# Performance work log

Hardware: AMD Instinct MI355X
Metric: run time of the kernel (lower is better)

## Reference

```python
import jax, jax.numpy as jnp
import numpy as np

H = 1024          # hidden_size
NH = 16           # num_heads = hidden_size // head_dim
DK = 64           # head_dim (key)
DV = 64           # head_v_dim
VDIM = 1024       # value_dim
DECAY_LR, GATE_LR, A_LR, V_LR = 64, 160, 64, 64
W_SCALE = -0.6065306597126334  # -exp(-0.5)
GN_EPS = 64 * 1e-5             # head_dim * norm_eps


def _lora(x, A, B, b, act):
    h = x @ A.T
    if act is not None:
        h = act(h)
    y = h @ B.T
    return y if b is None else y + b


def setup_inputs() -> dict:
    key = jax.random.key(0)
    ks = iter(jax.random.split(key, 40))
    def n(shape, s=0.02):
        return jax.random.normal(next(ks), shape, dtype=jnp.float32) * s
    inp = {
        'hidden_states': jax.random.normal(next(ks), (8, 2048, H), jnp.float32),
        'v_first': jax.random.normal(next(ks), (8, 2048, VDIM), jnp.float32),
        'x_r': n((1, 1, H), 0.5), 'x_w': n((1, 1, H), 0.5), 'x_k': n((1, 1, H), 0.5),
        'x_v': n((1, 1, H), 0.5), 'x_a': n((1, 1, H), 0.5), 'x_g': n((1, 1, H), 0.5),
        'k_k': 0.71 + n((H,), 0.05),
        'k_a': 1.02 + n((H,), 0.05),
        'r_k': -0.04 + n((NH, DK), 0.05),
        'W_r': n((H, H)), 'W_k': n((H, H)), 'W_v': n((VDIM, H)), 'W_o': n((H, VDIM)),
        'w_lora_A': n((DECAY_LR, H)), 'w_lora_B': n((H, DECAY_LR)), 'w_lora_b': n((H,), 0.5) - 4.0,
        'a_lora_A': n((A_LR, H)), 'a_lora_B': n((H, A_LR)), 'a_lora_b': n((H,), 0.1),
        'v_lora_A': n((V_LR, H)), 'v_lora_B': n((VDIM, V_LR)), 'v_lora_b': 0.73 + n((VDIM,), 0.1),
        'g_lora_A': n((GATE_LR, H)), 'g_lora_B': n((VDIM, GATE_LR)),
        'gn_w': jnp.ones((VDIM,), jnp.float32), 'gn_b': jnp.zeros((VDIM,), jnp.float32),
    }
    return inp


def reference(hidden_states, v_first, x_r, x_w, x_k, x_v, x_a, x_g, k_k, k_a, r_k,
              W_r, W_k, W_v, W_o, w_lora_A, w_lora_B, w_lora_b,
              a_lora_A, a_lora_B, a_lora_b, v_lora_A, v_lora_B, v_lora_b,
              g_lora_A, g_lora_B, gn_w, gn_b):
    x = hidden_states
    B_, T, _ = x.shape
    # token shift: delta[t] = x[t-1] - x[t], x[-1] = 0
    shifted = jnp.pad(x, ((0, 0), (1, 0), (0, 0)))[:, :T]
    delta = shifted - x
    xr = x + delta * x_r; xw = x + delta * x_w; xk = x + delta * x_k
    xv = x + delta * x_v; xa = x + delta * x_a; xg = x + delta * x_g

    r = xr @ W_r.T
    w = W_SCALE * jax.nn.sigmoid(_lora(xw, w_lora_A, w_lora_B, w_lora_b, jnp.tanh))  # log-decay in (-e^-0.5, 0)
    k = xk @ W_k.T
    v = xv @ W_v.T
    v = v + (v_first - v) * jax.nn.sigmoid(_lora(xv, v_lora_A, v_lora_B, v_lora_b, None))  # layer_idx != 0
    a = jax.nn.sigmoid(_lora(xa, a_lora_A, a_lora_B, a_lora_b, None))
    g = _lora(xg, g_lora_A, g_lora_B, None, jax.nn.sigmoid)

    kk = (k * k_k).reshape(B_, T, NH, DK)
    kk = kk / jnp.maximum(jnp.linalg.norm(kk, axis=-1, keepdims=True), 1e-12)  # l2 norm per head
    k = k * (1.0 + (a - 1.0) * k_a)

    rh = r.reshape(B_, T, NH, DK)
    wh = w.reshape(B_, T, NH, DK)
    kh = k.reshape(B_, T, NH, DK)
    vh = v.reshape(B_, T, NH, DV)
    ah = -kk                               # delta-rule 'a' (removal direction)
    bh = kk * a.reshape(B_, T, NH, DK)     # delta-rule 'b' (write direction)

    def step(S, inputs):
        # S: [B, H, DK, DV]; inputs each [B, H, D]
        r_t, w_t, k_t, v_t, a_t, b_t = inputs
        sa = jnp.einsum('bhk,bhkv->bhv', a_t, S)
        S = S * jnp.exp(w_t)[..., None] \
            + jnp.einsum('bhk,bhv->bhkv', b_t, sa) \
            + jnp.einsum('bhk,bhv->bhkv', k_t, v_t)
        o_t = jnp.einsum('bhk,bhkv->bhv', r_t, S)
        return S, o_t

    seq = tuple(jnp.moveaxis(t, 1, 0) for t in (rh, wh, kh, vh, ah, bh))  # [T,B,H,D]
    S0 = jnp.zeros((B_, NH, DK, DV), dtype=x.dtype)
    _, o = jax.lax.scan(step, S0, seq)
    o = jnp.moveaxis(o, 0, 1)  # [B, T, NH, DV]

    # GroupNorm with num_groups = num_heads over value_dim channels == per-head LayerNorm (no per-head affine)
    mu = o.mean(-1, keepdims=True)
    var = o.var(-1, keepdims=True)
    on = ((o - mu) / jnp.sqrt(var + GN_EPS)).reshape(B_, T, VDIM) * gn_w + gn_b

    bonus = ((rh * kh * r_k).sum(-1, keepdims=True) * vh).reshape(B_, T, VDIM)
    out = ((on + bonus) * g) @ W_o.T
    return out
```

## Files before the change

### kernel.cpp

```cpp
#include <hip/hip_runtime.h>
#include <hip/hip_bf16.h>


#define DEVI __device__ __forceinline__

constexpr int TSEQ = 2048;
constexpr int HID  = 1024;
constexpr int BTOT = 16384;
constexpr int CCH  = 32;
constexpr int NCH  = TSEQ / CCH;
constexpr int L4N  = 352;
constexpr float W_SCALE = -0.6065306597126334f;
constexpr float GN_EPS  = 6.4e-4f;

using s16x8  = __attribute__((ext_vector_type(8))) short;
using f32x4v = __attribute__((ext_vector_type(4))) float;

DEVI float4 ld4(const float* p) { return *reinterpret_cast<const float4*>(p); }
DEVI void   st4(float* p, float4 v) { *reinterpret_cast<float4*>(p) = v; }
DEVI float  sigf(float x) { return 1.0f / (1.0f + __expf(-x)); }
DEVI unsigned short bfr(float f) {
    unsigned int u = __float_as_uint(f);
    return (unsigned short)((u + 0x7fffu + ((u >> 16) & 1u)) >> 16);
}
DEVI float bff(unsigned short s) { return __uint_as_float(((unsigned int)s) << 16); }
DEVI unsigned int pk2(float lo, float hi) {
    return ((unsigned int)bfr(hi) << 16) | (unsigned int)bfr(lo);
}
DEVI void up8(uint4 u, float* f) {
    f[0]=bff((unsigned short)(u.x & 0xffffu)); f[1]=bff((unsigned short)(u.x >> 16));
    f[2]=bff((unsigned short)(u.y & 0xffffu)); f[3]=bff((unsigned short)(u.y >> 16));
    f[4]=bff((unsigned short)(u.z & 0xffffu)); f[5]=bff((unsigned short)(u.z >> 16));
    f[6]=bff((unsigned short)(u.w & 0xffffu)); f[7]=bff((unsigned short)(u.w >> 16));
}
DEVI f32x4v MF(s16x8 a, s16x8 b, f32x4v c) {
    return __builtin_amdgcn_mfma_f32_16x16x32_bf16(a, b, c, 0, 0, 0);
}
DEVI void gl16(const void* g, void* l) {
    __builtin_amdgcn_global_load_lds(
        (const __attribute__((address_space(1))) unsigned int*)g,
        (__attribute__((address_space(3))) unsigned int*)l, 16, 0, 0);
}
DEVI void gl4(const void* g, void* l) {
    __builtin_amdgcn_global_load_lds(
        (const __attribute__((address_space(1))) unsigned int*)g,
        (__attribute__((address_space(3))) unsigned int*)l, 4, 0, 0);
}

struct CastArgs {
    const float* src[12];
    unsigned short* dst[12];
    int start4[13];
};
__global__ __launch_bounds__(256) void cast_all_kernel(CastArgs a) {
    int i4 = blockIdx.x * 256 + threadIdx.x;
    if (i4 >= a.start4[12]) return;
    int seg = 0;
#pragma unroll
    for (int s = 1; s < 12; s++) seg += (i4 >= a.start4[s]) ? 1 : 0;
    int off = (i4 - a.start4[seg]) * 4;
    float4 v = ld4(a.src[seg] + off);
    ushort4 o; o.x = bfr(v.x); o.y = bfr(v.y); o.z = bfr(v.z); o.w = bfr(v.w);
    *reinterpret_cast<ushort4*>(a.dst[seg] + off) = o;
}

__global__ __launch_bounds__(256) void proj3_kernel(
        const float* __restrict__ x,
        const float* __restrict__ cr, const float* __restrict__ ck,
        const float* __restrict__ cv,
        const unsigned short* __restrict__ Wr, const unsigned short* __restrict__ Wk,
        const unsigned short* __restrict__ Wv,
        unsigned short* __restrict__ Ro, unsigned short* __restrict__ Ko,
        unsigned short* __restrict__ Vo) {
    __shared__ __align__(16) unsigned short As[3][64 * 32];
    __shared__ __align__(16) unsigned short Bs[3][128 * 32];
    const int tid = threadIdx.x;
    const int w = tid >> 6, l = tid & 63;
    const int bm = blockIdx.x * 64, bn = blockIdx.y * 128;
    const int wm = w >> 1, wn = w & 1;
    const int lr = l & 15, lq = l >> 4, lk = lq * 8;

    f32x4v acc[3][2][4];
#pragma unroll
    for (int p = 0; p < 3; p++)
#pragma unroll
        for (int i = 0; i < 2; i++)
#pragma unroll
            for (int j = 0; j < 4; j++)
#pragma unroll
                for (int q = 0; q < 4; q++) acc[p][i][j][q] = 0.f;

    const float* cvs[3] = {cr, ck, cv};
    const unsigned short* Ws[3] = {Wr, Wk, Wv};

    for (int k0 = 0; k0 < HID; k0 += 32) {
        {
            const int row = tid >> 2, kp = (tid & 3) * 8;
            const int gr = bm + row;
            const float* xp = x + (size_t)gr * HID + k0 + kp;
            float4 x0 = ld4(xp), x1 = ld4(xp + 4);
            float4 p0 = make_float4(0.f, 0.f, 0.f, 0.f), p1 = p0;
            if ((gr & (TSEQ - 1)) != 0) { p0 = ld4(xp - HID); p1 = ld4(xp - HID + 4); }
            float xb[8] = {x0.x, x0.y, x0.z, x0.w, x1.x, x1.y, x1.z, x1.w};
            float dx[8] = {p0.x - x0.x, p0.y - x0.y, p0.z - x0.z, p0.w - x0.w,
                           p1.x - x1.x, p1.y - x1.y, p1.z - x1.z, p1.w - x1.w};
#pragma unroll
            for (int p = 0; p < 3; p++) {
                float4 c0 = ld4(cvs[p] + k0 + kp), c1 = ld4(cvs[p] + k0 + kp + 4);
                float cc[8] = {c0.x, c0.y, c0.z, c0.w, c1.x, c1.y, c1.z, c1.w};
                uint4 u;
                u.x = pk2(fmaf(dx[0], cc[0], xb[0]), fmaf(dx[1], cc[1], xb[1]));
                u.y = pk2(fmaf(dx[2], cc[2], xb[2]), fmaf(dx[3], cc[3], xb[3]));
                u.z = pk2(fmaf(dx[4], cc[4], xb[4]), fmaf(dx[5], cc[5], xb[5]));
                u.w = pk2(fmaf(dx[6], cc[6], xb[6]), fmaf(dx[7], cc[7], xb[7]));
                *reinterpret_cast<uint4*>(&As[p][row * 32 + kp]) = u;
            }
        }
#pragma unroll
        for (int p = 0; p < 3; p++)
#pragma unroll
            for (int c = 0; c < 2; c++) {
                int idx = c * 256 + tid;
                int rw = idx >> 2, kp2 = (idx & 3) * 8;
                gl16(Ws[p] + (size_t)(bn + rw) * HID + k0 + kp2,
                     &Bs[p][c * 2048 + w * 512]);
            }
        __syncthreads();
#pragma unroll
        for (int p = 0; p < 3; p++) {
            s16x8 af[2], bf4[4];
#pragma unroll
            for (int i = 0; i < 2; i++)
                af[i] = *reinterpret_cast<const s16x8*>(
                    &As[p][(wm * 32 + i * 16 + lr) * 32 + lk]);
#pragma unroll
            for (int j = 0; j < 4; j++)
                bf4[j] = *reinterpret_cast<const s16x8*>(
                    &Bs[p][(wn * 64 + j * 16 + lr) * 32 + lk]);
#pragma unroll
            for (int i = 0; i < 2; i++)
#pragma unroll
                for (int j = 0; j < 4; j++)
                    acc[p][i][j] = MF(af[i], bf4[j], acc[p][i][j]);
        }
        __syncthreads();
    }

    unsigned short* dsts[3] = {Ro, Ko, Vo};
#pragma unroll
    for (int p = 0; p < 3; p++)
#pragma unroll
        for (int i = 0; i < 2; i++)
#pragma unroll
            for (int j = 0; j < 4; j++)
#pragma unroll
                for (int q = 0; q < 4; q++) {
                    const int grow = bm + wm * 32 + i * 16 + lq * 4 + q;
                    const int gcol = bn + wn * 64 + j * 16 + lr;
                    dsts[p][(size_t)grow * HID + gcol] = bfr(acc[p][i][j][q]);
                }
}

__global__ __launch_bounds__(256) void lora4_kernel(
        const float* __restrict__ x,
        const float* __restrict__ cv_, const float* __restrict__ cw_,
        const float* __restrict__ ca_, const float* __restrict__ cg_,
        const unsigned short* __restrict__ LW, unsigned short* __restrict__ H1) {
    __shared__ __align__(16) unsigned short As[4][64 * 32];
    __shared__ __align__(16) unsigned short Bs[L4N * 32];
    const int tid = threadIdx.x;
    const int w = tid >> 6, l = tid & 63;
    const int lr = l & 15, lq = l >> 4, lk = lq * 8;
    const int bm = blockIdx.x * 64;
    const float* cvs[4] = {cv_, cw_, ca_, cg_};

    f32x4v acc[22];
#pragma unroll
    for (int j = 0; j < 22; j++)
#pragma unroll
        for (int q = 0; q < 4; q++) acc[j][q] = 0.f;

    for (int k0 = 0; k0 < HID; k0 += 32) {
        {
            const int row = tid >> 2, kp = (tid & 3) * 8;
            const int gr = bm + row;
            const float* xp = x + (size_t)gr * HID + k0 + kp;
            float4 x0 = ld4(xp), x1 = ld4(xp + 4);
            float4 p0 = make_float4(0.f, 0.f, 0.f, 0.f), p1 = p0;
            if ((gr & (TSEQ - 1)) != 0) { p0 = ld4(xp - HID); p1 = ld4(xp - HID + 4); }
            float xb[8] = {x0.x, x0.y, x0.z, x0.w, x1.x, x1.y, x1.z, x1.w};
            float dx[8] = {p0.x - x0.x, p0.y - x0.y, p0.z - x0.z, p0.w - x0.w,
                           p1.x - x1.x, p1.y - x1.y, p1.z - x1.z, p1.w - x1.w};
#pragma unroll
            for (int p = 0; p < 4; p++) {
                float4 c0 = ld4(cvs[p] + k0 + kp), c1 = ld4(cvs[p] + k0 + kp + 4);
                float cc[8] = {c0.x, c0.y, c0.z, c0.w, c1.x, c1.y, c1.z, c1.w};
                uint4 u;
                u.x = pk2(fmaf(dx[0], cc[0], xb[0]), fmaf(dx[1], cc[1], xb[1]));
                u.y = pk2(fmaf(dx[2], cc[2], xb[2]), fmaf(dx[3], cc[3], xb[3]));
                u.z = pk2(fmaf(dx[4], cc[4], xb[4]), fmaf(dx[5], cc[5], xb[5]));
                u.w = pk2(fmaf(dx[6], cc[6], xb[6]), fmaf(dx[7], cc[7], xb[7]));
                *reinterpret_cast<uint4*>(&As[p][row * 32 + kp]) = u;
            }
        }
#pragma unroll
        for (int c = 0; c < 6; c++) {
            int idx = c * 256 + tid;
            if (idx < L4N * 4) {
                gl16(LW + (size_t)(idx >> 2) * HID + (idx & 3) * 8 + k0,
                     (char*)&Bs[0] + (c * 256 + w * 64) * 16);
            }
        }
        __syncthreads();
        s16x8 af[4];
#pragma unroll
        for (int p = 0; p < 4; p++)
            af[p] = *reinterpret_cast<const s16x8*>(&As[p][(w * 16 + lr) * 32 + lk]);
#pragma unroll
        for (int j = 0; j < 22; j++) {
            const int grp = (j < 4) ? 0 : (j < 8) ? 1 : (j < 12) ? 2 : 3;
            s16x8 bf = *reinterpret_cast<const s16x8*>(&Bs[(j * 16 + lr) * 32 + lk]);
            acc[j] = MF(af[grp], bf, acc[j]);
        }
        __syncthreads();
    }

#pragma unroll
    for (int j = 0; j < 22; j++)
#pragma unroll
        for (int q = 0; q < 4; q++) {
            const int grow = bm + w * 16 + lq * 4 + q;
            const int gcol = j * 16 + lr;
            float d = acc[j][q];
            if (j >= 4 && j < 8) d = tanhf(d);
            else if (j >= 12) d = sigf(d);
            H1[(size_t)grow * L4N + gcol] = bfr(d);
        }
}

__global__ __launch_bounds__(256) void stage2_kernel(
        const unsigned short* __restrict__ H1,
        const unsigned short* __restrict__ vB16, const unsigned short* __restrict__ wB16,
        const unsigned short* __restrict__ aB16,
        const float* __restrict__ vb, const float* __restrict__ wb,
        const float* __restrict__ ab,
        unsigned short* __restrict__ Vout, unsigned short* __restrict__ Wout,
        unsigned short* __restrict__ Aout,
        const unsigned short* __restrict__ aux1, const float* __restrict__ aux2) {
    const int z = blockIdx.z;
    const unsigned short* Bw = (z == 0) ? vB16 : (z == 1) ? wB16 : aB16;
    const float* bias = (z == 0) ? vb : (z == 1) ? wb : ab;
    unsigned short* Cout = (z == 0) ? Vout : (z == 1) ? Wout : Aout;
    const int aoff = z * 64;
    __shared__ __align__(16) unsigned short As[128 * 32];
    __shared__ __align__(16) unsigned short Bs[128 * 32];
    const int tid = threadIdx.x;
    const int w = tid >> 6, l = tid & 63;
    const int bm = blockIdx.x * 128, bn = blockIdx.y * 128;
    const int wm = w >> 1, wn = w & 1;
    const int lr = l & 15, lk = (l >> 4) * 8;

    f32x4v acc[4][4];
#pragma unroll
    for (int i = 0; i < 4; i++)
#pragma unroll
        for (int j = 0; j < 4; j++)
#pragma unroll
            for (int q = 0; q < 4; q++) acc[i][j][q] = 0.f;

    for (int k0 = 0; k0 < 64; k0 += 32) {
#pragma unroll
        for (int c = 0; c < 2; c++) {
            int idx = c * 256 + tid;
            int row = idx >> 2, kp = (idx & 3) * 8;
            gl16(H1 + (size_t)(bm + row) * L4N + aoff + k0 + kp,
                 &As[c * 2048 + w * 512]);
        }
#pragma unroll
        for (int c = 0; c < 2; c++) {
            int idx = c * 256 + tid;
            int row = idx >> 2, kp = (idx & 3) * 8;
            gl16(Bw + (size_t)(bn + row) * 64 + k0 + kp, &Bs[c * 2048 + w * 512]);
        }
        __syncthreads();
        s16x8 afx[4], bfx[4];
#pragma unroll
        for (int i = 0; i < 4; i++)
            afx[i] = *reinterpret_cast<const s16x8*>(&As[(wm * 64 + i * 16 + lr) * 32 + lk]);
#pragma unroll
        for (int j = 0; j < 4; j++)
            bfx[j] = *reinterpret_cast<const s16x8*>(&Bs[(wn * 64 + j * 16 + lr) * 32 + lk]);
#pragma unroll
        for (int i = 0; i < 4; i++)
#pragma unroll
            for (int j = 0; j < 4; j++)
                acc[i][j] = MF(afx[i], bfx[j], acc[i][j]);
        __syncthreads();
    }

#pragma unroll
    for (int i = 0; i < 4; i++) {
        const int grow0 = bm + wm * 64 + i * 16 + (l >> 4) * 4;
#pragma unroll
        for (int j = 0; j < 4; j++) {
            const int gcol = bn + wn * 64 + j * 16 + lr;
            const float bsv = bias[gcol];
#pragma unroll
            for (int q = 0; q < 4; q++) {
                const int grow = grow0 + q;
                float d = acc[i][j][q];
                if (z == 0) {
                    float v0 = bff(aux1[(size_t)grow * HID + gcol]);
                    d = fmaf(aux2[(size_t)grow * HID + gcol] - v0, sigf(d + bsv), v0);
                } else if (z == 1) {
                    d = W_SCALE * sigf(d + bsv);
                } else {
                    d = sigf(d + bsv);
                }
                Cout[(size_t)grow * HID + gcol] = bfr(d);
            }
        }
    }
}

template<int BM, int BN, int MODE, bool OUTBF>
__global__ __launch_bounds__(256) void mgemm(
        const unsigned short* __restrict__ Ab, const unsigned short* __restrict__ Bw,
        void* Cout, int N, int K, int lda,
        const float* __restrict__ bias,
        const unsigned short* aux1, const float* __restrict__ aux2) {
    constexpr int BK = 32;
    constexpr int WM_ = (BN == 128) ? 2 : 4;
    constexpr int WN_ = (BN == 128) ? 2 : 1;
    constexpr int WTM = BM / WM_, WTN = BN / WN_;
    constexpr int MF_ = WTM / 16, NF = WTN / 16;
    constexpr int ACALLS = (BM * BK) / 2048;
    constexpr int BCALLS = (BN * BK) / 2048;
    __shared__ __align__(16) unsigned short As[BM * BK];
    __shared__ __align__(16) unsigned short Bs[BN * BK];
    const int tid = threadIdx.x;
    const int w = tid >> 6, l = tid & 63;
    const int bm = blockIdx.x * BM, bn = blockIdx.y * BN;
    const int wm = w / WN_, wn = w % WN_;
    const int lr = l & 15, lk = (l >> 4) * 8;

    f32x4v acc[MF_][NF];
#pragma unroll
    for (int i = 0; i < MF_; i++)
#pragma unroll
        for (int j = 0; j < NF; j++)
#pragma unroll
            for (int q = 0; q < 4; q++) acc[i][j][q] = 0.f;

    for (int k0 = 0; k0 < K; k0 += BK) {
#pragma unroll
        for (int c = 0; c < ACALLS; c++) {
            int idx = c * 256 + tid;
            int row = idx >> 2, kp = (idx & 3) * 8;
            gl16(Ab + (size_t)(bm + row) * lda + k0 + kp, &As[c * 2048 + w * 512]);
        }
#pragma unroll
        for (int c = 0; c < BCALLS; c++) {
            int idx = c * 256 + tid;
            int row = idx >> 2, kp = (idx & 3) * 8;
            int gc = bn + row; if (gc > N - 1) gc = N - 1;
            gl16(Bw + (size_t)gc * K + k0 + kp, &Bs[c * 2048 + w * 512]);
        }
        __syncthreads();
        s16x8 afx[MF_], bfx[NF];
#pragma unroll
        for (int i = 0; i < MF_; i++)
            afx[i] = *reinterpret_cast<const s16x8*>(&As[(wm * WTM + i * 16 + lr) * BK + lk]);
#pragma unroll
        for (int j = 0; j < NF; j++)
            bfx[j] = *reinterpret_cast<const s16x8*>(&Bs[(wn * WTN + j * 16 + lr) * BK + lk]);
#pragma unroll
        for (int i = 0; i < MF_; i++)
#pragma unroll
            for (int j = 0; j < NF; j++)
                acc[i][j] = __builtin_amdgcn_mfma_f32_16x16x32_bf16(
                    afx[i], bfx[j], acc[i][j], 0, 0, 0);
        __syncthreads();
    }

#pragma unroll
    for (int i = 0; i < MF_; i++) {
        const int grow0 = bm + wm * WTM + i * 16 + (l >> 4) * 4;
#pragma unroll
        for (int j = 0; j < NF; j++) {
            const int gcol = bn + wn * WTN + j * 16 + lr;
            if (gcol >= N) continue;
#pragma unroll
            for (int q = 0; q < 4; q++) {
                const int grow = grow0 + q;
                float d = acc[i][j][q];
                if (OUTBF) ((unsigned short*)Cout)[(size_t)grow * N + gcol] = bfr(d);
                else       ((float*)Cout)[(size_t)grow * N + gcol] = d;
            }
        }
    }
}

__global__ __launch_bounds__(64) void cprep_kernel(
        unsigned short* __restrict__ K16, unsigned short* __restrict__ A16,
        unsigned short* __restrict__ R16, unsigned short* __restrict__ KK16,
        const unsigned short* __restrict__ W16,
        const float* __restrict__ kkc, const float* __restrict__ kac,
        const float* __restrict__ rkw,
        float* __restrict__ SB, float* __restrict__ Ed,
        unsigned short* __restrict__ MvH, unsigned short* __restrict__ MvL) {
    __shared__ __align__(16) unsigned short sA[32][64], sB[32][64], sK[32][64];
    __shared__ __align__(16) unsigned short AtT[64][40];
    __shared__ __align__(16) float Mab[32][36];
    __shared__ __align__(16) unsigned short MnvH[32][40], MnvL[32][40];
    __shared__ __align__(16) unsigned short MakTH[32][40], MakTL[32][40];
    const int bid = blockIdx.x;
    const int bh = bid >> 6, ch = bid & 63;
    const int bb = bh >> 4, hh = bh & 15;
    const int l = threadIdx.x;
    const int chn = hh * 64 + l;
    const float kkcv = kkc[chn], kacv = kac[chn], rkv = rkw[chn];
    const size_t cbase = ((size_t)(bb * TSEQ) + ch * CCH) * HID + hh * 64;
    size_t off = cbase + l;
    float cw = 0.f, er = 1.f;
    for (int i = 0; i < CCH; i++, off += HID) {
        const float k = bff(K16[off]);
        const float a = bff(A16[off]);
        const float r = bff(R16[off]);
        const float wv = bff(W16[off]);
        const float kr = k * kkcv;
        float ss = kr * kr;
        ss += __shfl_xor(ss, 1);  ss += __shfl_xor(ss, 2);
        ss += __shfl_xor(ss, 4);  ss += __shfl_xor(ss, 8);
        ss += __shfl_xor(ss, 16); ss += __shfl_xor(ss, 32);
        const float inv = 1.0f / fmaxf(sqrtf(ss), 1e-12f);
        const float kk = kr * inv;
        const float b  = kk * a;
        const float kn = k * fmaf(a - 1.0f, kacv, 1.0f);
        float s3 = r * kn * rkv;
        s3 += __shfl_xor(s3, 1);  s3 += __shfl_xor(s3, 2);
        s3 += __shfl_xor(s3, 4);  s3 += __shfl_xor(s3, 8);
        s3 += __shfl_xor(s3, 16); s3 += __shfl_xor(s3, 32);
        if (l == 0) SB[(size_t)bh * TSEQ + ch * CCH + i] = s3;
        const float cwp = cw; cw += wv;
        const float ea = __expf(cwp), ei = __expf(-cw);
        er = __expf(cw);
        const unsigned short At = bfr(-kk * ea);
        const unsigned short Bt = bfr(b * ei);
        const unsigned short Kt = bfr(kn * ei);
        A16[off] = Bt;
        K16[off] = Kt;
        R16[off] = bfr(r * er);
        sA[i][l] = At; sB[i][l] = Bt; sK[i][l] = Kt;
        AtT[l][i] = At;
    }
    Ed[((size_t)bh * NCH + ch) * 64 + l] = er;
    __syncthreads();
    const int lr = l & 15, lq = l >> 4;
    f32x4v z4; z4[0] = z4[1] = z4[2] = z4[3] = 0.f;
#pragma unroll
    for (int mi = 0; mi < 2; mi++)
#pragma unroll
        for (int ni = 0; ni < 2; ni++) {
            s16x8 a0 = *reinterpret_cast<const s16x8*>(&sA[mi * 16 + lr][lq * 8]);
            s16x8 a1 = *reinterpret_cast<const s16x8*>(&sA[mi * 16 + lr][32 + lq * 8]);
            s16x8 b0 = *reinterpret_cast<const s16x8*>(&sB[ni * 16 + lr][lq * 8]);
            s16x8 b1 = *reinterpret_cast<const s16x8*>(&sB[ni * 16 + lr][32 + lq * 8]);
            s16x8 k0 = *reinterpret_cast<const s16x8*>(&sK[ni * 16 + lr][lq * 8]);
            s16x8 k1 = *reinterpret_cast<const s16x8*>(&sK[ni * 16 + lr][32 + lq * 8]);
            f32x4v m  = MF(a1, b1, MF(a0, b0, z4));
            f32x4v mk = MF(a1, k1, MF(a0, k0, z4));
#pragma unroll
            for (int q = 0; q < 4; q++) {
                int r = mi * 16 + lq * 4 + q, cc2 = ni * 16 + lr;
                Mab[r][cc2] = (cc2 < r) ? m[q] : 0.f;
                float vv = (cc2 < r) ? mk[q] : 0.f;
                unsigned short h = bfr(vv);
                MakTH[cc2][r] = h;
                MakTL[cc2][r] = bfr(vv - bff(h));
            }
        }
    __syncthreads();
    const int j = l & 31;
    float m[32];
#pragma unroll
    for (int i = 0; i < 32; i++) m[i] = (i == j) ? 1.f : 0.f;
#pragma unroll
    for (int i = 1; i < 32; i++) {
        float p0 = 0.f, p1 = 0.f, p2 = 0.f, p3 = 0.f;
#pragma unroll
        for (int k4_ = 0; k4_ < 32; k4_ += 4) {
            if (k4_ >= i) break;
            float4 L4 = *reinterpret_cast<const float4*>(&Mab[i][k4_]);
            p0 = fmaf(L4.x, m[k4_ + 0], p0);
            if (k4_ + 1 < i) p1 = fmaf(L4.y, m[k4_ + 1], p1);
            if (k4_ + 2 < i) p2 = fmaf(L4.z, m[k4_ + 2], p2);
            if (k4_ + 3 < i) p3 = fmaf(L4.w, m[k4_ + 3], p3);
        }
        m[i] += (p0 + p1) + (p2 + p3);
    }
    if (l < 32) {
#pragma unroll
        for (int i = 0; i < 32; i++) {
            unsigned short h = bfr(m[i]);
            MnvH[i][j] = h;
            MnvL[i][j] = bfr(m[i] - bff(h));
        }
    }
    __syncthreads();
    {
        unsigned short* dH = MvH + (size_t)(bh * NCH + ch) * 1024;
        unsigned short* dL = MvL + (size_t)(bh * NCH + ch) * 1024;
#pragma unroll
        for (int mi = 0; mi < 2; mi++) {
            s16x8 ah = *reinterpret_cast<const s16x8*>(&MnvH[mi * 16 + lr][lq * 8]);
            s16x8 al = *reinterpret_cast<const s16x8*>(&MnvL[mi * 16 + lr][lq * 8]);
#pragma unroll
            for (int n = 0; n < 4; n++) {
                s16x8 bt = *reinterpret_cast<const s16x8*>(&AtT[n * 16 + lr][lq * 8]);
                f32x4v am = MF(al, bt, MF(ah, bt, z4));
#pragma unroll
                for (int q = 0; q < 4; q++)
                    KK16[cbase + (size_t)(mi * 16 + lq * 4 + q) * HID + n * 16 + lr]
                        = bfr(am[q]);
            }
#pragma unroll
            for (int n = 0; n < 2; n++) {
                s16x8 mh = *reinterpret_cast<const s16x8*>(&MakTH[n * 16 + lr][lq * 8]);
                s16x8 ml = *reinterpret_cast<const s16x8*>(&MakTL[n * 16 + lr][lq * 8]);
                f32x4v lm = MF(ah, ml, MF(al, mh, MF(ah, mh, z4)));
#pragma unroll
                for (int q = 0; q < 4; q++) {
                    const int r = mi * 16 + lq * 4 + q, cc = n * 16 + lr;
                    unsigned short h = bfr(lm[q]);
                    dH[r * 32 + cc] = h;
                    dL[r * 32 + cc] = bfr(lm[q] - bff(h));
                }
            }
        }
    }
}

__global__ __launch_bounds__(256) void recchunk_kernel(
        const unsigned short* __restrict__ AMG, const unsigned short* __restrict__ BtG,
        const unsigned short* __restrict__ KtG, const unsigned short* __restrict__ RtG,
        const unsigned short* __restrict__ V16, const float* __restrict__ Ed,
        const unsigned short* __restrict__ LMH, const unsigned short* __restrict__ LML,
        unsigned short* __restrict__ Ob16) {
    __shared__ __align__(16) unsigned short stT[2][4][CCH][64];
    __shared__ __align__(16) unsigned short stMh[2][32][32], stMl[2][32][32];
    __shared__ __align__(16) unsigned short stV[2][CCH][16];
    __shared__ __align__(16) float stEd[2][64];
    __shared__ __align__(16) unsigned short Shi[16][74], Slo[16][74];
    __shared__ __align__(16) unsigned short BtT[64][42], KtT[64][42];
    __shared__ __align__(16) unsigned short VT[16][42];
    __shared__ __align__(16) unsigned short MrkH[32][42], MrkL[32][42];
    __shared__ __align__(16) unsigned short MrbH[32][42], MrbL[32][42];
    __shared__ __align__(16) unsigned short SATh[16][42], SATl[16][42];

    const int bid = blockIdx.x;
    const int vq = bid >> 7, bh = bid & 127;
    const int tid = threadIdx.x;
    const int w = tid >> 6, l = tid & 63;
    const int lr = l & 15, lq = l >> 4;
    const int bb = bh >> 4, hh = bh & 15;
    const size_t rowoff = ((size_t)bb * TSEQ) * HID + hh * 64;
    const int mi = w >> 1, ni = w & 1;

    const int r8 = l >> 3, ck = l & 7;
    const int swz8 = (ck ^ r8) * 8;

    auto STAGE = [&](int buf, int cn) {
        if (cn >= NCH) return;
        const size_t cb = rowoff + (size_t)(cn * CCH) * HID;
        const unsigned short* srcs[4] = {AMG, BtG, KtG, RtG};
        const unsigned short* T = srcs[w];
#pragma unroll
        for (int c = 0; c < 4; c++)
            gl16(T + cb + (size_t)(c * 8 + r8) * HID + swz8, &stT[buf][w][c * 8][0]);
        if (w == 0) {
            gl16(V16 + cb + (size_t)(l >> 1) * HID + vq * 16 + (l & 1) * 8,
                 &stV[buf][0][0]);
            gl4(Ed + ((size_t)bh * NCH + cn) * 64 + l, &stEd[buf][0]);
        } else if (w == 1) {
#pragma unroll
            for (int c = 0; c < 2; c++)
                gl16(LMH + (size_t)(bh * NCH + cn) * 1024 + c * 512 + l * 8,
                     (char*)&stMh[buf][0][0] + c * 1024);
        } else if (w == 2) {
#pragma unroll
            for (int c = 0; c < 2; c++)
                gl16(LML + (size_t)(bh * NCH + cn) * 1024 + c * 512 + l * 8,
                     (char*)&stMl[buf][0][0] + c * 1024);
        }
    };

    for (int idx = tid; idx < 16 * 74; idx += 256) {
        ((unsigned short*)Shi)[idx] = 0;
        ((unsigned short*)Slo)[idx] = 0;
    }
    STAGE(0, 0);
    asm volatile("s_waitcnt vmcnt(0)" ::: "memory");
    __syncthreads();

    auto fragT = [&](int bf, int tn, int rbase, int kb) -> s16x8 {
        int row = rbase + lr;
        int chv = ((kb >> 3) + lq) ^ (row & 7);
        return *reinterpret_cast<const s16x8*>(
            (const char*)&stT[bf][tn][0][0] + row * 128 + chv * 16);
    };
    auto fragS = [&](const unsigned short (*Sx)[74], int kb) -> s16x8 {
        return *reinterpret_cast<const s16x8*>(&Sx[lr][kb + lq * 8]);
    };
    auto frag42 = [&](const unsigned short (*T)[42], int rbase) -> s16x8 {
        return *reinterpret_cast<const s16x8*>(&T[rbase + lr][lq * 8]);
    };

    f32x4v Sacc;
#pragma unroll
    for (int q = 0; q < 4; q++) Sacc[q] = 0.f;
    f32x4v z4; z4[0] = z4[1] = z4[2] = z4[3] = 0.f;

    int buf = 0;
    for (int c = 0; c < NCH; c++) {
        STAGE(buf ^ 1, c + 1);
        {
            const int tt = tid & 31, g8 = tid >> 5;
            const int ch = g8 ^ (tt & 7);
            uint4 bu = *reinterpret_cast<const uint4*>(&stT[buf][1][tt][ch * 8]);
            uint4 ku = *reinterpret_cast<const uint4*>(&stT[buf][2][tt][ch * 8]);
            unsigned int bw[4] = {bu.x, bu.y, bu.z, bu.w};
            unsigned int kw[4] = {ku.x, ku.y, ku.z, ku.w};
#pragma unroll
            for (int e = 0; e < 4; e++) {
                BtT[g8 * 8 + 2 * e][tt]     = (unsigned short)(bw[e] & 0xffffu);
                BtT[g8 * 8 + 2 * e + 1][tt] = (unsigned short)(bw[e] >> 16);
                KtT[g8 * 8 + 2 * e][tt]     = (unsigned short)(kw[e] & 0xffffu);
                KtT[g8 * 8 + 2 * e + 1][tt] = (unsigned short)(kw[e] >> 16);
            }
            if (g8 < 4) {
                ushort4 vu = *reinterpret_cast<const ushort4*>(&stV[buf][tt][g8 * 4]);
                VT[g8 * 4 + 0][tt] = vu.x; VT[g8 * 4 + 1][tt] = vu.y;
                VT[g8 * 4 + 2][tt] = vu.z; VT[g8 * 4 + 3][tt] = vu.w;
            }
        }
        __syncthreads();
        f32x4v oac = z4;
        if (ni == 0) {
            s16x8 rt0 = fragT(buf, 3, mi * 16, 0), rt1 = fragT(buf, 3, mi * 16, 32);
            s16x8 sh0 = fragS(Shi, 0), sh1 = fragS(Shi, 32);
            s16x8 sl0 = fragS(Slo, 0), sl1 = fragS(Slo, 32);
            oac = MF(rt1, sl1, MF(rt0, sl0, MF(rt1, sh1, MF(rt0, sh0, z4))));
#pragma unroll
            for (int n = 0; n < 2; n++) {
                s16x8 kt0 = fragT(buf, 2, n * 16, 0), kt1 = fragT(buf, 2, n * 16, 32);
                s16x8 bt0 = fragT(buf, 1, n * 16, 0), bt1 = fragT(buf, 1, n * 16, 32);
                f32x4v mrk = MF(rt1, kt1, MF(rt0, kt0, z4));
                f32x4v mrb = MF(rt1, bt1, MF(rt0, bt0, z4));
#pragma unroll
                for (int q = 0; q < 4; q++) {
                    const int r = mi * 16 + lq * 4 + q, cc = n * 16 + lr;
                    float vv = (cc <= r) ? mrk[q] : 0.f;
                    unsigned short h = bfr(vv);
                    MrkH[r][cc] = h; MrkL[r][cc] = bfr(vv - bff(h));
                    vv = (cc <= r) ? mrb[q] : 0.f; h = bfr(vv);
                    MrbH[r][cc] = h; MrbL[r][cc] = bfr(vv - bff(h));
                }
            }
        } else {
            s16x8 am0 = fragT(buf, 0, mi * 16, 0), am1 = fragT(buf, 0, mi * 16, 32);
            s16x8 sh0 = fragS(Shi, 0), sh1 = fragS(Shi, 32);
            s16x8 sl0 = fragS(Slo, 0), sl1 = fragS(Slo, 32);
            s16x8 vt0 = frag42(VT, 0);
            s16x8 lmh = *reinterpret_cast<const s16x8*>(&stMh[buf][mi * 16 + lr][lq * 8]);
            s16x8 lml = *reinterpret_cast<const s16x8*>(&stMl[buf][mi * 16 + lr][lq * 8]);
            f32x4v sat = MF(sl1, am1, MF(sl0, am0, MF(sh1, am1, MF(sh0, am0, z4))));
            sat = MF(vt0, lml, MF(vt0, lmh, sat));
#pragma unroll
            for (int q = 0; q < 4; q++) {
                const int r = lq * 4 + q, cc = mi * 16 + lr;
                unsigned short h = bfr(sat[q]);
                SATh[r][cc] = h;
                SATl[r][cc] = bfr(sat[q] - bff(h));
            }
        }
        __syncthreads();
        if (ni == 0) {
            s16x8 vt0 = frag42(VT, 0);
            oac = MF(frag42(MrkL, mi * 16), vt0,
                     MF(frag42(MrkH, mi * 16), vt0, oac));
            s16x8 sath = frag42(SATh, 0), satl = frag42(SATl, 0);
            s16x8 rbh = frag42(MrbH, mi * 16), rbl = frag42(MrbL, mi * 16);
            oac = MF(rbl, sath, MF(rbh, satl, MF(rbh, sath, oac)));
#pragma unroll
            for (int q = 0; q < 4; q++) {
                const int t = c * CCH + mi * 16 + lq * 4 + q;
                Ob16[rowoff + (size_t)t * HID + vq * 16 + lr] = bfr(oac[q]);
            }
        }
        {
            s16x8 sath = frag42(SATh, 0), satl = frag42(SATl, 0);
            s16x8 btf = frag42(BtT, w * 16);
            s16x8 ktf = frag42(KtT, w * 16);
            s16x8 vta = frag42(VT, 0);
            const float ed = stEd[buf][w * 16 + lr];
            Sacc = MF(sath, btf, Sacc);
            Sacc = MF(satl, btf, Sacc);
            Sacc = MF(vta, ktf, Sacc);
#pragma unroll
            for (int q = 0; q < 4; q++) {
                Sacc[q] *= ed;
                unsigned short h = bfr(Sacc[q]);
                Shi[lq * 4 + q][w * 16 + lr] = h;
                Slo[lq * 4 + q][w * 16 + lr] = bfr(Sacc[q] - bff(h));
            }
        }
        asm volatile("s_waitcnt vmcnt(0)" ::: "memory");
        __syncthreads();
        buf ^= 1;
    }
}

__global__ __launch_bounds__(256) void stats_kernel(
        const unsigned short* __restrict__ O16, float* __restrict__ MS) {
    const int row = blockIdx.x;
    const int tid = threadIdx.x;
    const int c = tid * 4;
    ushort4 ou = *reinterpret_cast<const ushort4*>(O16 + (size_t)row * HID + c);
    float o[4] = {bff(ou.x), bff(ou.y), bff(ou.z), bff(ou.w)};
    float s1 = o[0] + o[1] + o[2] + o[3];
    float s2 = o[0]*o[0] + o[1]*o[1] + o[2]*o[2] + o[3]*o[3];
#pragma unroll
    for (int m = 1; m < 16; m <<= 1) {
        s1 += __shfl_xor(s1, m); s2 += __shfl_xor(s2, m);
    }
    if ((tid & 15) == 0) {
        const int hh = tid >> 4;
        const float mu = s1 * (1.0f / 64.0f);
        const float var = s2 * (1.0f / 64.0f) - mu * mu;
        float2 v; v.x = mu; v.y = rsqrtf(var + GN_EPS);
        *reinterpret_cast<float2*>(MS + (size_t)row * 32 + hh * 2) = v;
    }
}

__global__ __launch_bounds__(256) void wogemm_kernel(
        const unsigned short* __restrict__ O16, const unsigned short* __restrict__ V16,
        const unsigned short* __restrict__ G16, const float* __restrict__ SB,
        const float* __restrict__ MS, const float* __restrict__ gnw,
        const float* __restrict__ gnb, const unsigned short* __restrict__ Wo,
        float* __restrict__ out) {
    __shared__ __align__(16) unsigned short As[128 * 32];
    __shared__ __align__(16) unsigned short Bs[128 * 32];
    const int tid = threadIdx.x;
    const int w = tid >> 6, l = tid & 63;
    const int bm = blockIdx.x * 128, bn = blockIdx.y * 128;
    const int wm = w >> 1, wn = w & 1;
    const int lr = l & 15, lk = (l >> 4) * 8;

    f32x4v acc[4][4];
#pragma unroll
    for (int i = 0; i < 4; i++)
#pragma unroll
        for (int j = 0; j < 4; j++)
#pragma unroll
            for (int q = 0; q < 4; q++) acc[i][j][q] = 0.f;

    for (int k0 = 0; k0 < HID; k0 += 32) {
#pragma unroll
        for (int c = 0; c < 2; c++) {
            int idx = c * 256 + tid;
            int row = idx >> 2, kp = (idx & 3) * 8;
            const int gr = bm + row;
            const size_t rb = (size_t)gr * HID + k0 + kp;
            uint4 ou = *reinterpret_cast<const uint4*>(O16 + rb);
            uint4 vu = *reinterpret_cast<const uint4*>(V16 + rb);
            uint4 gu = *reinterpret_cast<const uint4*>(G16 + rb);
            float o8[8], v8[8], g8[8];
            up8(ou, o8); up8(vu, v8); up8(gu, g8);
            const int hh = (k0 + kp) >> 6;
            float2 ms = *reinterpret_cast<const float2*>(MS + (size_t)gr * 32 + hh * 2);
            const float s3 = SB[((size_t)(gr >> 11) * 16 + hh) * TSEQ + (gr & (TSEQ - 1))];
            float4 w0 = ld4(gnw + k0 + kp), w1 = ld4(gnw + k0 + kp + 4);
            float4 b0 = ld4(gnb + k0 + kp), b1 = ld4(gnb + k0 + kp + 4);
            float wn8[8] = {w0.x, w0.y, w0.z, w0.w, w1.x, w1.y, w1.z, w1.w};
            float bn8[8] = {b0.x, b0.y, b0.z, b0.w, b1.x, b1.y, b1.z, b1.w};
            float y[8];
#pragma unroll
            for (int e = 0; e < 8; e++)
                y[e] = (fmaf((o8[e] - ms.x) * ms.y, wn8[e], bn8[e]) + s3 * v8[e]) * g8[e];
            uint4 u;
            u.x = pk2(y[0], y[1]); u.y = pk2(y[2], y[3]);
            u.z = pk2(y[4], y[5]); u.w = pk2(y[6], y[7]);
            *reinterpret_cast<uint4*>(&As[idx * 8]) = u;
        }
#pragma unroll
        for (int c = 0; c < 2; c++) {
            int idx = c * 256 + tid;
            int row = idx >> 2, kp = (idx & 3) * 8;
            gl16(Wo + (size_t)(bn + row) * HID + k0 + kp, &Bs[c * 2048 + w * 512]);
        }
        __syncthreads();
        s16x8 afx[4], bfx[4];
#pragma unroll
        for (int i = 0; i < 4; i++)
            afx[i] = *reinterpret_cast<const s16x8*>(&As[(wm * 64 + i * 16 + lr) * 32 + lk]);
#pragma unroll
        for (int j = 0; j < 4; j++)
            bfx[j] = *reinterpret_cast<const s16x8*>(&Bs[(wn * 64 + j * 16 + lr) * 32 + lk]);
#pragma unroll
        for (int i = 0; i < 4; i++)
#pragma unroll
            for (int j = 0; j < 4; j++)
                acc[i][j] = MF(afx[i], bfx[j], acc[i][j]);
        __syncthreads();
    }

#pragma unroll
    for (int i = 0; i < 4; i++) {
        const int grow0 = bm + wm * 64 + i * 16 + (l >> 4) * 4;
#pragma unroll
        for (int j = 0; j < 4; j++) {
            const int gcol = bn + wn * 64 + j * 16 + lr;
#pragma unroll
            for (int q = 0; q < 4; q++)
                out[(size_t)(grow0 + q) * HID + gcol] = acc[i][j][q];
        }
    }
}

extern "C" void kernel_launch(void* const* d_in, const int* in_sizes, int n_in,
                              void* d_out, int out_size, void* d_ws, size_t ws_size,
                              hipStream_t stream) {
    const float* x   = (const float*)d_in[0];
    const float* vf  = (const float*)d_in[1];
    const float* x_r = (const float*)d_in[2];
    const float* x_w = (const float*)d_in[3];
    const float* x_k = (const float*)d_in[4];
    const float* x_v = (const float*)d_in[5];
    const float* x_a = (const float*)d_in[6];
    const float* x_g = (const float*)d_in[7];
    const float* k_k = (const float*)d_in[8];
    const float* k_a = (const float*)d_in[9];
    const float* r_k = (const float*)d_in[10];
    const float* W_r = (const float*)d_in[11];
    const float* W_k = (const float*)d_in[12];
    const float* W_v = (const float*)d_in[13];
    const float* W_o = (const float*)d_in[14];
    const float* wA  = (const float*)d_in[15];
    const float* wB  = (const float*)d_in[16];
    const float* wb  = (const float*)d_in[17];
    const float* aA  = (const float*)d_in[18];
    const float* aB  = (const float*)d_in[19];
    const float* ab  = (const float*)d_in[20];
    const float* vA  = (const float*)d_in[21];
    const float* vB  = (const float*)d_in[22];
    const float* vb  = (const float*)d_in[23];
    const float* gA  = (const float*)d_in[24];
    const float* gB  = (const float*)d_in[25];
    const float* gnw = (const float*)d_in[26];
    const float* gnb = (const float*)d_in[27];
    float* out = (float*)d_out;

    float* ws = (float*)d_ws;
    const size_t SZ = (size_t)BTOT * HID;
    const size_t HH = (size_t)HID * HID;
    float*          REG  = ws;
    unsigned short* P    = (unsigned short*)(ws + SZ);
    unsigned short* R16  = P;
    unsigned short* K16  = P + 1 * SZ;
    unsigned short* V16  = P + 2 * SZ;
    unsigned short* A16  = P + 3 * SZ;
    unsigned short* KK16 = P + 4 * SZ;
    unsigned short* H1   = P + 5 * SZ;
    unsigned short* WR   = H1 + (size_t)BTOT * L4N;
    unsigned short* Wr16 = WR;
    unsigned short* Wk16 = WR + 1 * HH;
    unsigned short* Wv16 = WR + 2 * HH;
    unsigned short* Wo16 = WR + 3 * HH;
    unsigned short* LW   = WR + 4 * HH;
    unsigned short* vB16 = LW + (size_t)L4N * HID;
    unsigned short* wB16 = vB16 + 65536;
    unsigned short* aB16 = wB16 + 65536;
    unsigned short* gB16 = aB16 + 65536;
    float*          SB   = (float*)(gB16 + 163840);
    float*          Ed   = SB + (size_t)128 * TSEQ;
    float*          MS   = Ed;
    unsigned short* W16   = (unsigned short*)REG;
    unsigned short* O16   = (unsigned short*)REG;
    unsigned short* LMHp  = (unsigned short*)(REG + 8 * 1024 * 1024);
    unsigned short* LMLp  = LMHp + (size_t)128 * NCH * 1024;
    unsigned short* G16   = (unsigned short*)(REG + 8 * 1024 * 1024);

    const dim3 blk(256);
    const dim3 gBig(128, 8);
    const dim3 gP3(BTOT / 64, 8);
    const unsigned short* nu = nullptr;
    const float* np = nullptr;

    CastArgs ca;
    const float* srcs[12] = {W_r, W_k, W_v, W_o, vA, wA, aA, gA, vB, wB, aB, gB};
    unsigned short* dsts[12] = {Wr16, Wk16, Wv16, Wo16,
                                LW, LW + 65536, LW + 131072, LW + 196608,
                                vB16, wB16, aB16, gB16};
    int cnts[12] = {(int)HH, (int)HH, (int)HH, (int)HH,
                    65536, 65536, 65536, 163840, 65536, 65536, 65536, 163840};
    int acc4 = 0;
    for (int s = 0; s < 12; s++) {
        ca.src[s] = srcs[s]; ca.dst[s] = dsts[s];
        ca.start4[s] = acc4;
        acc4 += cnts[s] / 4;
    }
    ca.start4[12] = acc4;
    cast_all_kernel<<<dim3((acc4 + 255) / 256), blk, 0, stream>>>(ca);

    proj3_kernel<<<gP3, blk, 0, stream>>>(
        x, x_r, x_k, x_v, Wr16, Wk16, Wv16, R16, K16, V16);
    lora4_kernel<<<dim3(BTOT / 64), blk, 0, stream>>>(
        x, x_v, x_w, x_a, x_g, LW, H1);
    stage2_kernel<<<dim3(128, 8, 3), blk, 0, stream>>>(
        H1, vB16, wB16, aB16, vb, wb, ab, V16, W16, A16, V16, vf);
    cprep_kernel<<<dim3(128 * NCH), dim3(64), 0, stream>>>(
        K16, A16, R16, KK16, W16, k_k, k_a, r_k, SB, Ed, LMHp, LMLp);
    recchunk_kernel<<<dim3(512), blk, 0, stream>>>(
        KK16, A16, K16, R16, V16, Ed, LMHp, LMLp, O16);
    mgemm<128,128,0,true><<<gBig, blk, 0, stream>>>(
        H1 + 192, gB16, G16, HID, 160, L4N, np, nu, np);
    stats_kernel<<<dim3(BTOT), blk, 0, stream>>>(O16, MS);
    wogemm_kernel<<<gBig, blk, 0, stream>>>(
        O16, V16, G16, SB, MS, gnw, gnb, Wo16, out);
    (void)in_sizes; (void)n_in; (void)out_size; (void)ws_size;
}
```

Baseline: 1.195 ms.

## Split chunk prep into row-wise prep and separate compose kernel

The chunk preparation kernel is split in two. The first kernel does the per-row scaling and writes the scaled At/Bt/Kt values to global memory (At now goes into KK16). The second kernel reads them back from global memory to build the intra-chunk matrices and the inverse. This cuts shared memory and register pressure per kernel so more blocks can run at once, at the cost of an extra launch and a global write and read of the chunk data.

Result: faster. 960.7 us (-19.6%).

```diff
diff --git a/kernel.cpp b/kernel.cpp
--- a/kernel.cpp
+++ b/kernel.cpp
@@ -401,27 +401,20 @@
     }
 }
 
-__global__ __launch_bounds__(64) void cprep_kernel(
+__global__ __launch_bounds__(64) void rowprep_kernel(
         unsigned short* __restrict__ K16, unsigned short* __restrict__ A16,
         unsigned short* __restrict__ R16, unsigned short* __restrict__ KK16,
         const unsigned short* __restrict__ W16,
         const float* __restrict__ kkc, const float* __restrict__ kac,
         const float* __restrict__ rkw,
-        float* __restrict__ SB, float* __restrict__ Ed,
-        unsigned short* __restrict__ MvH, unsigned short* __restrict__ MvL) {
-    __shared__ __align__(16) unsigned short sA[32][64], sB[32][64], sK[32][64];
-    __shared__ __align__(16) unsigned short AtT[64][40];
-    __shared__ __align__(16) float Mab[32][36];
-    __shared__ __align__(16) unsigned short MnvH[32][40], MnvL[32][40];
-    __shared__ __align__(16) unsigned short MakTH[32][40], MakTL[32][40];
+        float* __restrict__ SB, float* __restrict__ Ed) {
     const int bid = blockIdx.x;
     const int bh = bid >> 6, ch = bid & 63;
     const int bb = bh >> 4, hh = bh & 15;
     const int l = threadIdx.x;
     const int chn = hh * 64 + l;
     const float kkcv = kkc[chn], kacv = kac[chn], rkv = rkw[chn];
-    const size_t cbase = ((size_t)(bb * TSEQ) + ch * CCH) * HID + hh * 64;
-    size_t off = cbase + l;
+    size_t off = ((size_t)(bb * TSEQ) + ch * CCH) * HID + chn;
     float cw = 0.f, er = 1.f;
     for (int i = 0; i < CCH; i++, off += HID) {
         const float k = bff(K16[off]);
@@ -445,29 +438,47 @@
         const float cwp = cw; cw += wv;
         const float ea = __expf(cwp), ei = __expf(-cw);
         er = __expf(cw);
-        const unsigned short At = bfr(-kk * ea);
-        const unsigned short Bt = bfr(b * ei);
-        const unsigned short Kt = bfr(kn * ei);
-        A16[off] = Bt;
-        K16[off] = Kt;
-        R16[off] = bfr(r * er);
-        sA[i][l] = At; sB[i][l] = Bt; sK[i][l] = Kt;
-        AtT[l][i] = At;
+        KK16[off] = bfr(-kk * ea);
+        A16[off]  = bfr(b * ei);
+        K16[off]  = bfr(kn * ei);
+        R16[off]  = bfr(r * er);
     }
     Ed[((size_t)bh * NCH + ch) * 64 + l] = er;
-    __syncthreads();
+}
+
+__global__ __launch_bounds__(64) void compose_kernel(
+        const unsigned short* __restrict__ BtG, const unsigned short* __restrict__ KtG,
+        unsigned short* __restrict__ KK16,
+        unsigned short* __restrict__ MvH, unsigned short* __restrict__ MvL) {
+    __shared__ __align__(16) unsigned short AtT[64][40];
+    __shared__ __align__(16) float Mab[32][36];
+    __shared__ __align__(16) unsigned short MakTH[32][40], MakTL[32][40];
+    __shared__ __align__(16) unsigned short MnvH[32][40], MnvL[32][40];
+    const int bid = blockIdx.x;
+    const int bh = bid >> 6, ch = bid & 63;
+    const int bb = bh >> 4, hh = bh & 15;
+    const size_t cbase = ((size_t)(bb * TSEQ) + ch * CCH) * HID + hh * 64;
+    const int l = threadIdx.x;
     const int lr = l & 15, lq = l >> 4;
+    for (int i = 0; i < 32; i++)
+        AtT[l][i] = KK16[cbase + (size_t)i * HID + l];
     f32x4v z4; z4[0] = z4[1] = z4[2] = z4[3] = 0.f;
 #pragma unroll
-    for (int mi = 0; mi < 2; mi++)
+    for (int mi = 0; mi < 2; mi++) {
+        s16x8 a0 = *reinterpret_cast<const s16x8*>(
+            KK16 + cbase + (size_t)(mi * 16 + lr) * HID + lq * 8);
+        s16x8 a1 = *reinterpret_cast<const s16x8*>(
+            KK16 + cbase + (size_t)(mi * 16 + lr) * HID + 32 + lq * 8);
 #pragma unroll
         for (int ni = 0; ni < 2; ni++) {
-            s16x8 a0 = *reinterpret_cast<const s16x8*>(&sA[mi * 16 + lr][lq * 8]);
-            s16x8 a1 = *reinterpret_cast<const s16x8*>(&sA[mi * 16 + lr][32 + lq * 8]);
-            s16x8 b0 = *reinterpret_cast<const s16x8*>(&sB[ni * 16 + lr][lq * 8]);
-            s16x8 b1 = *reinterpret_cast<const s16x8*>(&sB[ni * 16 + lr][32 + lq * 8]);
-            s16x8 k0 = *reinterpret_cast<const s16x8*>(&sK[ni * 16 + lr][lq * 8]);
-            s16x8 k1 = *reinterpret_cast<const s16x8*>(&sK[ni * 16 + lr][32 + lq * 8]);
+            s16x8 b0 = *reinterpret_cast<const s16x8*>(
+                BtG + cbase + (size_t)(ni * 16 + lr) * HID + lq * 8);
+            s16x8 b1 = *reinterpret_cast<const s16x8*>(
+                BtG + cbase + (size_t)(ni * 16 + lr) * HID + 32 + lq * 8);
+            s16x8 k0 = *reinterpret_cast<const s16x8*>(
+                KtG + cbase + (size_t)(ni * 16 + lr) * HID + lq * 8);
+            s16x8 k1 = *reinterpret_cast<const s16x8*>(
+                KtG + cbase + (size_t)(ni * 16 + lr) * HID + 32 + lq * 8);
             f32x4v m  = MF(a1, b1, MF(a0, b0, z4));
             f32x4v mk = MF(a1, k1, MF(a0, k0, z4));
 #pragma unroll
@@ -480,6 +491,7 @@
                 MakTL[cc2][r] = bfr(vv - bff(h));
             }
         }
+    }
     __syncthreads();
     const int j = l & 31;
     float m[32];
@@ -919,8 +931,10 @@
         x, x_v, x_w, x_a, x_g, LW, H1);
     stage2_kernel<<<dim3(128, 8, 3), blk, 0, stream>>>(
         H1, vB16, wB16, aB16, vb, wb, ab, V16, W16, A16, V16, vf);
-    cprep_kernel<<<dim3(128 * NCH), dim3(64), 0, stream>>>(
-        K16, A16, R16, KK16, W16, k_k, k_a, r_k, SB, Ed, LMHp, LMLp);
+    rowprep_kernel<<<dim3(128 * NCH), dim3(64), 0, stream>>>(
+        K16, A16, R16, KK16, W16, k_k, k_a, r_k, SB, Ed);
+    compose_kernel<<<dim3(128 * NCH), dim3(64), 0, stream>>>(
+        A16, K16, KK16, LMHp, LMLp);
     recchunk_kernel<<<dim3(512), blk, 0, stream>>>(
         KK16, A16, K16, R16, V16, Ed, LMHp, LMLp, O16);
     mgemm<128,128,0,true><<<gBig, blk, 0, stream>>>(
```
